# Kernel tuning notes

Hardware: AMD Instinct MI355X
Metric: run time of the kernel (lower is better)

The kernel has to match this reference:

```python
import jax, jax.numpy as jnp
import numpy as np

N = 50000
E = 800000
F_IN = 128
H1, C1 = 8, 32   # conv1: heads=8, out_channels=32 -> concat 256
H2, C2 = 1, 32   # conv2: heads=1, out_channels=32
NEG_SLOPE = 0.2


def setup_inputs() -> dict:
    key = jax.random.key(0)
    ks = jax.random.split(key, 10)
    x = jax.random.normal(ks[0], (N, F_IN), dtype=jnp.float32)
    edge_index = jax.random.randint(ks[1], (2, E), 0, N, dtype=jnp.int64)
    s1 = 1.0 / np.sqrt(F_IN)
    s2 = 1.0 / np.sqrt(H1 * C1)
    return {
        "x": x,
        "edge_index": edge_index,
        "W1": jax.random.normal(ks[2], (F_IN, H1 * C1), dtype=jnp.float32) * s1,
        "b1": jnp.zeros((H1 * C1,), dtype=jnp.float32),
        "att_src1": jax.random.normal(ks[3], (1, H1, C1), dtype=jnp.float32) * s1,
        "att_dst1": jax.random.normal(ks[4], (1, H1, C1), dtype=jnp.float32) * s1,
        "W2": jax.random.normal(ks[5], (H1 * C1, H2 * C2), dtype=jnp.float32) * s2,
        "b2": jnp.zeros((H2 * C2,), dtype=jnp.float32),
        "att_src2": jax.random.normal(ks[6], (1, H2, C2), dtype=jnp.float32) * s2,
        "att_dst2": jax.random.normal(ks[7], (1, H2, C2), dtype=jnp.float32) * s2,
    }


def _gat_conv(x, src, tgt, W, b, att_src, att_dst, heads, ch):
    n = x.shape[0]
    h = (x @ W).reshape(n, heads, ch)                      # [N,H,C]
    a_s = jnp.sum(h * att_src, axis=-1)                    # [N,H]
    a_d = jnp.sum(h * att_dst, axis=-1)                    # [N,H]
    e = jax.nn.leaky_relu(a_s[src] + a_d[tgt], NEG_SLOPE)  # [E',H]
    m = jax.ops.segment_max(e, tgt, num_segments=n)        # per-target max
    e = jnp.exp(e - m[tgt])
    denom = jax.ops.segment_sum(e, tgt, num_segments=n)
    alpha = e / denom[tgt]                                 # edge softmax over in-edges
    msg = h[src] * alpha[:, :, None]                       # [E',H,C]
    out = jax.ops.segment_sum(msg, tgt, num_segments=n)    # scatter-add at targets
    return out.reshape(n, heads * ch) + b


def reference(x, edge_index, W1, b1, att_src1, att_dst1, W2, b2, att_src2, att_dst2):
    n = x.shape[0]
    # PyG GATConv adds self-loops inside each conv; same augmented edge set both layers.
    loops = jnp.arange(n, dtype=edge_index.dtype)
    src = jnp.concatenate([edge_index[0], loops])  # message source j
    tgt = jnp.concatenate([edge_index[1], loops])  # message target i
    h = _gat_conv(x, src, tgt, W1, b1, att_src1, att_dst1, H1, C1)
    h = jax.nn.elu(h)
    h = _gat_conv(h, src, tgt, W2, b2, att_src2, att_dst2, H2, C2)
    return jax.nn.elu(h)
```

## Files before the change

kernel.cpp:

```cpp
#include <hip/hip_runtime.h>
#include <hip/hip_fp16.h>
#include <cmath>

#define NNODES 50000
#define NEDGES 800000
#define ETOT   (NEDGES + NNODES)
#define FIN    128
#define NH1    8
#define NC1    32
#define HC1    256
#define NC2    32

#define NBUCK  ((NNODES + 63) / 64)
#define BCAP   1536
#define EPB    4096

using half8 = __attribute__((ext_vector_type(8))) _Float16;
using f32x4 = __attribute__((ext_vector_type(4))) float;

__device__ __forceinline__ float lrelu(float x) { return x > 0.f ? x : 0.2f * x; }

#define NB_CASTX ((NNODES * FIN / 4 + 255) / 256)
#define NB_W1    ((FIN * HC1 + 255) / 256)
#define NB_W2    ((HC1 * NC2 + 255) / 256)
#define NB_P1    ((ETOT + EPB - 1) / EPB)

__global__ void __launch_bounds__(256) prep_k(const float* __restrict__ x,
        __half* __restrict__ xh, const float* __restrict__ W1, __half* __restrict__ W1t,
        const float* __restrict__ W2, __half* __restrict__ W2t,
        const int* __restrict__ ei, int* __restrict__ bcnt, unsigned* __restrict__ pairs) {
    __shared__ int lcnt[NBUCK];
    __shared__ int gbase[NBUCK];
    int b = blockIdx.x;
    if (b < NB_CASTX) {
        int i = b * 256 + threadIdx.x;
        if (i < NNODES * FIN / 4) {
            float4 v = ((const float4*)x)[i];
            __half2 a = __floats2half2_rn(v.x, v.y);
            __half2 c = __floats2half2_rn(v.z, v.w);
            uint2 w; w.x = *(unsigned*)&a; w.y = *(unsigned*)&c;
            ((uint2*)xh)[i] = w;
        }
        return;
    }
    b -= NB_CASTX;
    if (b < NB_W1) {
        int i = b * 256 + threadIdx.x;
        if (i < FIN * HC1) {
            int k = i / HC1, n = i - k * HC1;
            W1t[(size_t)n * FIN + k] = __float2half(W1[i]);
        }
        return;
    }
    b -= NB_W1;
    if (b < NB_W2) {
        int i = b * 256 + threadIdx.x;
        if (i < HC1 * NC2) {
            int k = i / NC2, n = i - k * NC2;
            W2t[(size_t)n * HC1 + k] = __float2half(W2[i]);
        }
        return;
    }
    b -= NB_W2;
    for (int i = threadIdx.x; i < NBUCK; i += 256) lcnt[i] = 0;
    __syncthreads();
    int e0 = b * EPB + threadIdx.x;
    int bk[16]; int rk[16]; unsigned pk[16];
#pragma unroll
    for (int k = 0; k < 16; ++k) {
        int e = e0 + k * 256;
        bk[k] = -1;
        if (e < ETOT) {
            int s, t;
            if (e < NEDGES) { s = ei[e]; t = ei[NEDGES + e]; } else { s = t = e - NEDGES; }
            int bb = t >> 6;
            bk[k] = bb;
            rk[k] = atomicAdd(&lcnt[bb], 1);
            pk[k] = ((unsigned)(t & 63) << 16) | (unsigned)s;
        }
    }
    __syncthreads();
    for (int i = threadIdx.x; i < NBUCK; i += 256) {
        int c = lcnt[i];
        gbase[i] = c ? atomicAdd(bcnt + i, c) : 0;
    }
    __syncthreads();
#pragma unroll
    for (int k = 0; k < 16; ++k) {
        if (bk[k] >= 0) {
            int pos = gbase[bk[k]] + rk[k];
            if (pos < BCAP) pairs[(size_t)bk[k] * BCAP + pos] = pk[k];
        }
    }
}

__global__ void __launch_bounds__(256) pass2_k(const unsigned* __restrict__ pairs,
        const int* __restrict__ bcnt, int* __restrict__ csr,
        int* __restrict__ rp_start, int* __restrict__ cntT) {
    int b = blockIdx.x;
    int nb = bcnt[b]; nb = nb < BCAP ? nb : BCAP;
    __shared__ int lcnt64[64];
    __shared__ int base64[64];
    __shared__ unsigned short binned[BCAP];
    if (threadIdx.x < 64) lcnt64[threadIdx.x] = 0;
    __syncthreads();
    unsigned ps[6]; int rks[6]; bool vld[6];
#pragma unroll
    for (int k = 0; k < 6; ++k) {
        int i = threadIdx.x + k * 256;
        vld[k] = i < nb;
        if (vld[k]) {
            unsigned p = pairs[(size_t)b * BCAP + i];
            ps[k] = p;
            rks[k] = atomicAdd(&lcnt64[p >> 16], 1);
        }
    }
    __syncthreads();
    if (threadIdx.x < 64) {
        int v = lcnt64[threadIdx.x];
        int inc = v;
#pragma unroll
        for (int ofs = 1; ofs < 64; ofs <<= 1) {
            int o = __shfl_up(inc, ofs, 64);
            if ((int)threadIdx.x >= ofs) inc += o;
        }
        base64[threadIdx.x] = inc - v;
    }
    __syncthreads();
#pragma unroll
    for (int k = 0; k < 6; ++k) {
        if (vld[k]) binned[base64[ps[k] >> 16] + rks[k]] = (unsigned short)(ps[k] & 0xFFFFu);
    }
    __syncthreads();
    for (int i = threadIdx.x; i < nb; i += 256)
        csr[(size_t)b * BCAP + i] = binned[i];
    if (threadIdx.x < 64) {
        int t = b * 64 + threadIdx.x;
        if (t < NNODES) {
            rp_start[t] = b * BCAP + base64[threadIdx.x];
            cntT[t] = lcnt64[threadIdx.x];
        }
    }
}

__global__ void __launch_bounds__(256) mgemm1_k(const __half* __restrict__ A,
        const __half* __restrict__ Bt, const float* __restrict__ att_s,
        const float* __restrict__ att_d, __half* __restrict__ C,
        float* __restrict__ as_, float* __restrict__ ad_) {
    const _Float16* Af = (const _Float16*)A;
    const _Float16* Bf = (const _Float16*)Bt;
    int wv = threadIdx.x >> 6, lane = threadIdx.x & 63;
    int r16 = lane & 15, kg = lane >> 4;
    int bm = blockIdx.x * 16;
    int arow = bm + r16; if (arow >= NNODES) arow = NNODES - 1;
    f32x4 acc[4] = {};
#pragma unroll
    for (int kt = 0; kt < FIN; kt += 32) {
        half8 a = *(const half8*)(Af + (size_t)arow * FIN + kt + kg * 8);
#pragma unroll
        for (int ct = 0; ct < 4; ++ct) {
            int col = wv * 64 + ct * 16 + r16;
            half8 b = *(const half8*)(Bf + (size_t)col * FIN + kt + kg * 8);
            acc[ct] = __builtin_amdgcn_mfma_f32_16x16x32_f16(a, b, acc[ct], 0, 0, 0);
        }
    }
#pragma unroll
    for (int ct = 0; ct < 4; ++ct)
#pragma unroll
        for (int r = 0; r < 4; ++r) {
            int orow = bm + kg * 4 + r;
            if (orow < NNODES)
                C[(size_t)orow * HC1 + wv * 64 + ct * 16 + r16] = __float2half(acc[ct][r]);
        }
#pragma unroll
    for (int P = 0; P < 2; ++P) {
        int head = 2 * wv + P;
        float ws0 = att_s[head * 32 + r16], ws1 = att_s[head * 32 + 16 + r16];
        float wd0 = att_d[head * 32 + r16], wd1 = att_d[head * 32 + 16 + r16];
        float sv[4], dv[4];
#pragma unroll
        for (int r = 0; r < 4; ++r) {
            sv[r] = acc[2 * P][r] * ws0 + acc[2 * P + 1][r] * ws1;
            dv[r] = acc[2 * P][r] * wd0 + acc[2 * P + 1][r] * wd1;
#pragma unroll
            for (int ofs = 1; ofs < 16; ofs <<= 1) {
                sv[r] += __shfl_xor(sv[r], ofs, 64);
                dv[r] += __shfl_xor(dv[r], ofs, 64);
            }
        }
#pragma unroll
        for (int r = 0; r < 4; ++r) {
            int orow = bm + kg * 4 + r;
            if (r16 == r && orow < NNODES) {
                as_[orow * NH1 + head] = sv[r];
                ad_[orow * NH1 + head] = dv[r];
            }
        }
    }
}

__global__ void __launch_bounds__(256) mgemm2_k(const __half* __restrict__ A,
        const __half* __restrict__ Bt, const float* __restrict__ att_s,
        const float* __restrict__ att_d, __half* __restrict__ C,
        float* __restrict__ as_, float* __restrict__ ad_) {
    const _Float16* Af = (const _Float16*)A;
    const _Float16* Bf = (const _Float16*)Bt;
    int wv = threadIdx.x >> 6, lane = threadIdx.x & 63;
    int r16 = lane & 15, kg = lane >> 4;
    int bm = blockIdx.x * 64 + wv * 16;
    int arow = bm + r16; if (arow >= NNODES) arow = NNODES - 1;
    f32x4 acc[2] = {};
#pragma unroll
    for (int kt = 0; kt < HC1; kt += 32) {
        half8 a = *(const half8*)(Af + (size_t)arow * HC1 + kt + kg * 8);
#pragma unroll
        for (int ct = 0; ct < 2; ++ct) {
            half8 b = *(const half8*)(Bf + (size_t)(ct * 16 + r16) * HC1 + kt + kg * 8);
            acc[ct] = __builtin_amdgcn_mfma_f32_16x16x32_f16(a, b, acc[ct], 0, 0, 0);
        }
    }
#pragma unroll
    for (int ct = 0; ct < 2; ++ct)
#pragma unroll
        for (int r = 0; r < 4; ++r) {
            int orow = bm + kg * 4 + r;
            if (orow < NNODES)
                C[(size_t)orow * NC2 + ct * 16 + r16] = __float2half(acc[ct][r]);
        }
    float ws0 = att_s[r16], ws1 = att_s[16 + r16];
    float wd0 = att_d[r16], wd1 = att_d[16 + r16];
    float sv[4], dv[4];
#pragma unroll
    for (int r = 0; r < 4; ++r) {
        sv[r] = acc[0][r] * ws0 + acc[1][r] * ws1;
        dv[r] = acc[0][r] * wd0 + acc[1][r] * wd1;
#pragma unroll
        for (int ofs = 1; ofs < 16; ofs <<= 1) {
            sv[r] += __shfl_xor(sv[r], ofs, 64);
            dv[r] += __shfl_xor(dv[r], ofs, 64);
        }
    }
#pragma unroll
    for (int r = 0; r < 4; ++r) {
        int orow = bm + kg * 4 + r;
        if (r16 == r && orow < NNODES) { as_[orow] = sv[r]; ad_[orow] = dv[r]; }
    }
}

__global__ void __launch_bounds__(256) gather1_k(const int* __restrict__ rp_start,
        const int* __restrict__ cntT, const int* __restrict__ csr,
        const __half* __restrict__ h, const float* __restrict__ as_,
        const float* __restrict__ ad_, const float* __restrict__ bias,
        __half* __restrict__ out) {
    int t = blockIdx.x * 4 + (threadIdx.x >> 6);
    int lane = threadIdx.x & 63;
    if (t >= NNODES) return;
    int hh = lane & 7;
    int hd = lane >> 3;
    float adv = ad_[t * NH1 + hh];
    int n = cntT[t];
    const int* cb = csr + rp_start[t];
    const uint2* h4 = (const uint2*)h;
    float4 acc = make_float4(0.f, 0.f, 0.f, 0.f);
    float dpart = 0.f;

    for (int i = 0; i < n; i += 8) {
        int ii = i + (lane >> 3);
        bool val = ii < n;
        int sj = cb[val ? ii : 0];
        float p = expf(lrelu(as_[sj * NH1 + hh] + adv));
        p = val ? p : 0.f;
        dpart += p;
        uint2 raw[8];
#pragma unroll
        for (int j = 0; j < 8; ++j) {
            int s = __shfl(sj, 8 * j, 64);
            raw[j] = h4[(size_t)s * 64 + lane];
        }
#pragma unroll
        for (int j = 0; j < 8; ++j) {
            float al = __shfl(p, 8 * j + hd, 64);
            float2 f0 = __half22float2(*(const __half2*)&raw[j].x);
            float2 f1 = __half22float2(*(const __half2*)&raw[j].y);
            acc.x += al * f0.x; acc.y += al * f0.y;
            acc.z += al * f1.x; acc.w += al * f1.y;
        }
    }
    dpart += __shfl_xor(dpart, 8, 64);
    dpart += __shfl_xor(dpart, 16, 64);
    dpart += __shfl_xor(dpart, 32, 64);
    float inv = __shfl(1.f / dpart, hd, 64);
    float4 bv = ((const float4*)bias)[lane];
    float4 r;
    r.x = acc.x * inv + bv.x; r.y = acc.y * inv + bv.y;
    r.z = acc.z * inv + bv.z; r.w = acc.w * inv + bv.w;
    r.x = r.x > 0.f ? r.x : expm1f(r.x);
    r.y = r.y > 0.f ? r.y : expm1f(r.y);
    r.z = r.z > 0.f ? r.z : expm1f(r.z);
    r.w = r.w > 0.f ? r.w : expm1f(r.w);
    __half2 p0 = __floats2half2_rn(r.x, r.y);
    __half2 p1 = __floats2half2_rn(r.z, r.w);
    uint2 w; w.x = *(unsigned*)&p0; w.y = *(unsigned*)&p1;
    ((uint2*)out)[(size_t)t * 64 + lane] = w;
}

__global__ void __launch_bounds__(256) gather2_k(const int* __restrict__ rp_start,
        const int* __restrict__ cntT, const int* __restrict__ csr,
        const __half* __restrict__ h, const float* __restrict__ as_,
        const float* __restrict__ ad_, const float* __restrict__ bias,
        float* __restrict__ out) {
    int t = blockIdx.x * 4 + (threadIdx.x >> 6);
    int lane = threadIdx.x & 63;
    if (t >= NNODES) return;
    int q = lane >> 3, f = lane & 7;
    float adv = ad_[t];
    int n = cntT[t];
    const int* cb = csr + rp_start[t];
    const uint2* h8 = (const uint2*)h;
    float4 acc = make_float4(0.f, 0.f, 0.f, 0.f);
    float dpart = 0.f;

    for (int i = 0; i < n; i += 8) {
        int ii = i + q;
        bool val = ii < n;
        int s = cb[val ? ii : 0];
        float p = expf(lrelu(as_[s] + adv));
        p = val ? p : 0.f;
        dpart += p;
        uint2 raw[8];
#pragma unroll
        for (int j = 0; j < 8; ++j) {
            int sj = __shfl(s, 8 * j, 64);
            raw[j] = h8[(size_t)sj * 8 + f];
        }
#pragma unroll
        for (int j = 0; j < 8; ++j) {
            float al = __shfl(p, 8 * j, 64);
            float2 f0 = __half22float2(*(const __half2*)&raw[j].x);
            float2 f1 = __half22float2(*(const __half2*)&raw[j].y);
            acc.x += al * f0.x; acc.y += al * f0.y;
            acc.z += al * f1.x; acc.w += al * f1.y;
        }
    }
    dpart += __shfl_xor(dpart, 8, 64);
    dpart += __shfl_xor(dpart, 16, 64);
    dpart += __shfl_xor(dpart, 32, 64);
    if (q == 0) {
        float inv = 1.f / dpart;
        float4 bv = ((const float4*)bias)[f];
        float4 r;
        r.x = acc.x * inv + bv.x; r.y = acc.y * inv + bv.y;
        r.z = acc.z * inv + bv.z; r.w = acc.w * inv + bv.w;
        r.x = r.x > 0.f ? r.x : expm1f(r.x);
        r.y = r.y > 0.f ? r.y : expm1f(r.y);
        r.z = r.z > 0.f ? r.z : expm1f(r.z);
        r.w = r.w > 0.f ? r.w : expm1f(r.w);
        ((float4*)out)[(size_t)t * 8 + f] = r;
    }
}

extern "C" void kernel_launch(void* const* d_in, const int* in_sizes, int n_in,
                              void* d_out, int out_size, void* d_ws, size_t ws_size,
                              hipStream_t stream) {
    const float* x    = (const float*)d_in[0];
    const int*   ei   = (const int*)d_in[1];
    const float* W1   = (const float*)d_in[2];
    const float* b1   = (const float*)d_in[3];
    const float* as1w = (const float*)d_in[4];
    const float* ad1w = (const float*)d_in[5];
    const float* W2   = (const float*)d_in[6];
    const float* b2   = (const float*)d_in[7];
    const float* as2w = (const float*)d_in[8];
    const float* ad2w = (const float*)d_in[9];
    float* out = (float*)d_out;

    float* ws = (float*)d_ws;
    size_t off = 0;
    __half* xh   = (__half*)(ws + off); off += (size_t)NNODES * FIN / 2;
    __half* h1h  = (__half*)(ws + off); off += (size_t)NNODES * HC1 / 2;
    __half* out1h= (__half*)(ws + off); off += (size_t)NNODES * HC1 / 2;
    __half* h2h  = (__half*)(ws + off); off += (size_t)NNODES * NC2 / 2;
    __half* W1t  = (__half*)(ws + off); off += (size_t)FIN * HC1 / 2;
    __half* W2t  = (__half*)(ws + off); off += (size_t)HC1 * NC2 / 2;
    float* as1  = ws + off; off += (size_t)NNODES * NH1;
    float* ad1  = ws + off; off += (size_t)NNODES * NH1;
    float* as2  = ws + off; off += NNODES;
    float* ad2  = ws + off; off += NNODES;
    unsigned* pairs = (unsigned*)(ws + off); off += (size_t)NBUCK * BCAP;
    int* csr      = (int*)(ws + off); off += (size_t)NBUCK * BCAP;
    int* bcnt     = (int*)(ws + off); off += NBUCK;
    int* rp_start = (int*)(ws + off); off += NNODES;
    int* cntT     = (int*)(ws + off); off += NNODES;

    hipMemsetAsync(bcnt, 0, (size_t)NBUCK * 4, stream);
    prep_k<<<NB_CASTX + NB_W1 + NB_W2 + NB_P1, 256, 0, stream>>>(
        x, xh, W1, W1t, W2, W2t, ei, bcnt, pairs);
    pass2_k<<<NBUCK, 256, 0, stream>>>(pairs, bcnt, csr, rp_start, cntT);

    mgemm1_k<<<(NNODES + 15) / 16, 256, 0, stream>>>(xh, W1t, as1w, ad1w, h1h, as1, ad1);
    gather1_k<<<(NNODES + 3) / 4, 256, 0, stream>>>(rp_start, cntT, csr, h1h, as1, ad1, b1, out1h);

    mgemm2_k<<<(NNODES + 63) / 64, 256, 0, stream>>>(out1h, W2t, as2w, ad2w, h2h, as2, ad2);
    gather2_k<<<(NNODES + 3) / 4, 256, 0, stream>>>(rp_start, cntT, csr, h2h, as2, ad2, b2, out);
}
```

Baseline: 208.7 us.

## Fuse x cast into GEMM1, merge CSR pass2 with GEMM1, prefetch gather indices

```diff
diff --git a/kernel.cpp b/kernel.cpp
--- a/kernel.cpp
+++ b/kernel.cpp
@@ -20,30 +20,16 @@
 
 __device__ __forceinline__ float lrelu(float x) { return x > 0.f ? x : 0.2f * x; }
 
-#define NB_CASTX ((NNODES * FIN / 4 + 255) / 256)
 #define NB_W1    ((FIN * HC1 + 255) / 256)
 #define NB_W2    ((HC1 * NC2 + 255) / 256)
 #define NB_P1    ((ETOT + EPB - 1) / EPB)
 
-__global__ void __launch_bounds__(256) prep_k(const float* __restrict__ x,
-        __half* __restrict__ xh, const float* __restrict__ W1, __half* __restrict__ W1t,
-        const float* __restrict__ W2, __half* __restrict__ W2t,
+__global__ void __launch_bounds__(256) prep_k(const float* __restrict__ W1,
+        __half* __restrict__ W1t, const float* __restrict__ W2, __half* __restrict__ W2t,
         const int* __restrict__ ei, int* __restrict__ bcnt, unsigned* __restrict__ pairs) {
     __shared__ int lcnt[NBUCK];
     __shared__ int gbase[NBUCK];
     int b = blockIdx.x;
-    if (b < NB_CASTX) {
-        int i = b * 256 + threadIdx.x;
-        if (i < NNODES * FIN / 4) {
-            float4 v = ((const float4*)x)[i];
-            __half2 a = __floats2half2_rn(v.x, v.y);
-            __half2 c = __floats2half2_rn(v.z, v.w);
-            uint2 w; w.x = *(unsigned*)&a; w.y = *(unsigned*)&c;
-            ((uint2*)xh)[i] = w;
-        }
-        return;
-    }
-    b -= NB_CASTX;
     if (b < NB_W1) {
         int i = b * 256 + threadIdx.x;
         if (i < FIN * HC1) {
@@ -94,74 +80,78 @@
     }
 }
 
-__global__ void __launch_bounds__(256) pass2_k(const unsigned* __restrict__ pairs,
+__global__ void __launch_bounds__(256) combo_k(const unsigned* __restrict__ pairs,
         const int* __restrict__ bcnt, int* __restrict__ csr,
-        int* __restrict__ rp_start, int* __restrict__ cntT) {
-    int b = blockIdx.x;
-    int nb = bcnt[b]; nb = nb < BCAP ? nb : BCAP;
+        int* __restrict__ rp_start, int* __restrict__ cntT,
+        const float* __restrict__ x, const __half* __restrict__ Bt,
+        const float* __restrict__ att_s, const float* __restrict__ att_d,
+        __half* __restrict__ C, float* __restrict__ as_, float* __restrict__ ad_) {
     __shared__ int lcnt64[64];
     __shared__ int base64[64];
     __shared__ unsigned short binned[BCAP];
-    if (threadIdx.x < 64) lcnt64[threadIdx.x] = 0;
-    __syncthreads();
-    unsigned ps[6]; int rks[6]; bool vld[6];
-#pragma unroll
-    for (int k = 0; k < 6; ++k) {
-        int i = threadIdx.x + k * 256;
-        vld[k] = i < nb;
-        if (vld[k]) {
-            unsigned p = pairs[(size_t)b * BCAP + i];
-            ps[k] = p;
-            rks[k] = atomicAdd(&lcnt64[p >> 16], 1);
-        }
-    }
-    __syncthreads();
-    if (threadIdx.x < 64) {
-        int v = lcnt64[threadIdx.x];
-        int inc = v;
-#pragma unroll
-        for (int ofs = 1; ofs < 64; ofs <<= 1) {
-            int o = __shfl_up(inc, ofs, 64);
-            if ((int)threadIdx.x >= ofs) inc += o;
-        }
-        base64[threadIdx.x] = inc - v;
-    }
-    __syncthreads();
-#pragma unroll
-    for (int k = 0; k < 6; ++k) {
-        if (vld[k]) binned[base64[ps[k] >> 16] + rks[k]] = (unsigned short)(ps[k] & 0xFFFFu);
-    }
-    __syncthreads();
-    for (int i = threadIdx.x; i < nb; i += 256)
-        csr[(size_t)b * BCAP + i] = binned[i];
-    if (threadIdx.x < 64) {
-        int t = b * 64 + threadIdx.x;
-        if (t < NNODES) {
-            rp_start[t] = b * BCAP + base64[threadIdx.x];
-            cntT[t] = lcnt64[threadIdx.x];
-        }
-    }
-}
-
-__global__ void __launch_bounds__(256) mgemm1_k(const __half* __restrict__ A,
-        const __half* __restrict__ Bt, const float* __restrict__ att_s,
-        const float* __restrict__ att_d, __half* __restrict__ C,
-        float* __restrict__ as_, float* __restrict__ ad_) {
-    const _Float16* Af = (const _Float16*)A;
+    if (blockIdx.x < NBUCK) {
+        int b = blockIdx.x;
+        int nb = bcnt[b]; nb = nb < BCAP ? nb : BCAP;
+        if (threadIdx.x < 64) lcnt64[threadIdx.x] = 0;
+        __syncthreads();
+        unsigned ps[6]; int rks[6]; bool vld[6];
+#pragma unroll
+        for (int k = 0; k < 6; ++k) {
+            int i = threadIdx.x + k * 256;
+            vld[k] = i < nb;
+            if (vld[k]) {
+                unsigned p = pairs[(size_t)b * BCAP + i];
+                ps[k] = p;
+                rks[k] = atomicAdd(&lcnt64[p >> 16], 1);
+            }
+        }
+        __syncthreads();
+        if (threadIdx.x < 64) {
+            int v = lcnt64[threadIdx.x];
+            int inc = v;
+#pragma unroll
+            for (int ofs = 1; ofs < 64; ofs <<= 1) {
+                int o = __shfl_up(inc, ofs, 64);
+                if ((int)threadIdx.x >= ofs) inc += o;
+            }
+            base64[threadIdx.x] = inc - v;
+        }
+        __syncthreads();
+#pragma unroll
+        for (int k = 0; k < 6; ++k) {
+            if (vld[k]) binned[base64[ps[k] >> 16] + rks[k]] = (unsigned short)(ps[k] & 0xFFFFu);
+        }
+        __syncthreads();
+        for (int i = threadIdx.x; i < nb; i += 256)
+            csr[(size_t)b * BCAP + i] = binned[i];
+        if (threadIdx.x < 64) {
+            int t = b * 64 + threadIdx.x;
+            if (t < NNODES) {
+                rp_start[t] = b * BCAP + base64[threadIdx.x];
+                cntT[t] = lcnt64[threadIdx.x];
+            }
+        }
+        return;
+    }
     const _Float16* Bf = (const _Float16*)Bt;
+    int blk = blockIdx.x - NBUCK;
     int wv = threadIdx.x >> 6, lane = threadIdx.x & 63;
     int r16 = lane & 15, kg = lane >> 4;
-    int bm = blockIdx.x * 16;
+    int bm = blk * 16;
     int arow = bm + r16; if (arow >= NNODES) arow = NNODES - 1;
     f32x4 acc[4] = {};
 #pragma unroll
     for (int kt = 0; kt < FIN; kt += 32) {
-        half8 a = *(const half8*)(Af + (size_t)arow * FIN + kt + kg * 8);
+        const float4* xr = (const float4*)(x + (size_t)arow * FIN + kt + kg * 8);
+        float4 f0 = xr[0], f1 = xr[1];
+        half8 a;
+        a[0] = (_Float16)f0.x; a[1] = (_Float16)f0.y; a[2] = (_Float16)f0.z; a[3] = (_Float16)f0.w;
+        a[4] = (_Float16)f1.x; a[5] = (_Float16)f1.y; a[6] = (_Float16)f1.z; a[7] = (_Float16)f1.w;
 #pragma unroll
         for (int ct = 0; ct < 4; ++ct) {
             int col = wv * 64 + ct * 16 + r16;
-            half8 b = *(const half8*)(Bf + (size_t)col * FIN + kt + kg * 8);
-            acc[ct] = __builtin_amdgcn_mfma_f32_16x16x32_f16(a, b, acc[ct], 0, 0, 0);
+            half8 bfr = *(const half8*)(Bf + (size_t)col * FIN + kt + kg * 8);
+            acc[ct] = __builtin_amdgcn_mfma_f32_16x16x32_f16(a, bfr, acc[ct], 0, 0, 0);
         }
     }
 #pragma unroll
@@ -264,17 +254,22 @@
     float4 acc = make_float4(0.f, 0.f, 0.f, 0.f);
     float dpart = 0.f;
 
+    int slot = lane >> 3;
+    bool val0 = slot < n;
+    int sj0 = cb[val0 ? slot : 0];
+    float a0 = as_[sj0 * NH1 + hh];
+
     for (int i = 0; i < n; i += 8) {
-        int ii = i + (lane >> 3);
-        bool val = ii < n;
-        int sj = cb[val ? ii : 0];
-        float p = expf(lrelu(as_[sj * NH1 + hh] + adv));
-        p = val ? p : 0.f;
+        int ii = i + 8 + slot;
+        bool val1 = ii < n;
+        int sj1 = cb[val1 ? ii : 0];
+        float a1 = as_[sj1 * NH1 + hh];
+        float p = val0 ? expf(lrelu(a0 + adv)) : 0.f;
         dpart += p;
         uint2 raw[8];
 #pragma unroll
         for (int j = 0; j < 8; ++j) {
-            int s = __shfl(sj, 8 * j, 64);
+            int s = __shfl(sj0, 8 * j, 64);
             raw[j] = h4[(size_t)s * 64 + lane];
         }
 #pragma unroll
@@ -285,6 +280,7 @@
             acc.x += al * f0.x; acc.y += al * f0.y;
             acc.z += al * f1.x; acc.w += al * f1.y;
         }
+        sj0 = sj1; a0 = a1; val0 = val1;
     }
     dpart += __shfl_xor(dpart, 8, 64);
     dpart += __shfl_xor(dpart, 16, 64);
@@ -320,17 +316,21 @@
     float4 acc = make_float4(0.f, 0.f, 0.f, 0.f);
     float dpart = 0.f;
 
+    bool val0 = q < n;
+    int sj0 = cb[val0 ? q : 0];
+    float a0 = as_[sj0];
+
     for (int i = 0; i < n; i += 8) {
-        int ii = i + q;
-        bool val = ii < n;
-        int s = cb[val ? ii : 0];
-        float p = expf(lrelu(as_[s] + adv));
-        p = val ? p : 0.f;
+        int ii = i + 8 + q;
+        bool val1 = ii < n;
+        int sj1 = cb[val1 ? ii : 0];
+        float a1 = as_[sj1];
+        float p = val0 ? expf(lrelu(a0 + adv)) : 0.f;
         dpart += p;
         uint2 raw[8];
 #pragma unroll
         for (int j = 0; j < 8; ++j) {
-            int sj = __shfl(s, 8 * j, 64);
+            int sj = __shfl(sj0, 8 * j, 64);
             raw[j] = h8[(size_t)sj * 8 + f];
         }
 #pragma unroll
@@ -341,6 +341,7 @@
             acc.x += al * f0.x; acc.y += al * f0.y;
             acc.z += al * f1.x; acc.w += al * f1.y;
         }
+        sj0 = sj1; a0 = a1; val0 = val1;
     }
     dpart += __shfl_xor(dpart, 8, 64);
     dpart += __shfl_xor(dpart, 16, 64);
@@ -376,7 +377,6 @@
 
     float* ws = (float*)d_ws;
     size_t off = 0;
-    __half* xh   = (__half*)(ws + off); off += (size_t)NNODES * FIN / 2;
     __half* h1h  = (__half*)(ws + off); off += (size_t)NNODES * HC1 / 2;
     __half* out1h= (__half*)(ws + off); off += (size_t)NNODES * HC1 / 2;
     __half* h2h  = (__half*)(ws + off); off += (size_t)NNODES * NC2 / 2;
@@ -393,11 +393,10 @@
     int* cntT     = (int*)(ws + off); off += NNODES;
 
     hipMemsetAsync(bcnt, 0, (size_t)NBUCK * 4, stream);
-    prep_k<<<NB_CASTX + NB_W1 + NB_W2 + NB_P1, 256, 0, stream>>>(
-        x, xh, W1, W1t, W2, W2t, ei, bcnt, pairs);
-    pass2_k<<<NBUCK, 256, 0, stream>>>(pairs, bcnt, csr, rp_start, cntT);
-
-    mgemm1_k<<<(NNODES + 15) / 16, 256, 0, stream>>>(xh, W1t, as1w, ad1w, h1h, as1, ad1);
+    prep_k<<<NB_W1 + NB_W2 + NB_P1, 256, 0, stream>>>(W1, W1t, W2, W2t, ei, bcnt, pairs);
+    combo_k<<<NBUCK + (NNODES + 15) / 16, 256, 0, stream>>>(
+        pairs, bcnt, csr, rp_start, cntT, x, W1t, as1w, ad1w, h1h, as1, ad1);
+
     gather1_k<<<(NNODES + 3) / 4, 256, 0, stream>>>(rp_start, cntT, csr, h1h, as1, ad1, b1, out1h);
 
     mgemm2_k<<<(NNODES + 63) / 64, 256, 0, stream>>>(out1h, W2t, as2w, ad2w, h2h, as2, ad2);
```

Result: faster. 198.2 us (-5.1%).
